# Kernel tuning notes

Hardware: AMD Instinct MI355X
Metric: run time of the kernel (lower is better)

The kernel has to match this reference:

```python
import jax, jax.numpy as jnp
import numpy as np

H, DK, DV, DM = 8, 64, 64, 512
B, LQ, LK = 8, 512, 1024
NEG = -1e30  # stand-in for -inf (avoids NaN under masking)


def setup_inputs() -> dict:
    key = jax.random.key(0)
    ks = jax.random.split(key, 12)
    s = 0.04  # ~xavier scale for 512x512
    return {
        "q": jax.random.normal(ks[0], (B, LQ, DM), jnp.float32),
        "k": jax.random.normal(ks[1], (B, LK, DM), jnp.float32),
        "v": jax.random.normal(ks[2], (B, LK, DM), jnp.float32),
        "w_qs": jax.random.normal(ks[3], (DM, H * DK), jnp.float32) * s,
        "w_ks": jax.random.normal(ks[4], (DM, H * DK), jnp.float32) * s,
        "w_vs": jax.random.normal(ks[5], (DM, H * DV), jnp.float32) * s,
        "w_fc": jax.random.normal(ks[6], (H * DV, DM), jnp.float32) * s,
        "key_mask": (jax.random.uniform(ks[7], (B, LQ, LK)) > 0.1).astype(jnp.float32),
        "query_mask": (jax.random.uniform(ks[8], (B, LQ, 1)) > 0.1).astype(jnp.float32),
        "mapping_mask": (jax.random.uniform(ks[9], (B, LQ, LK)) > 0.1).astype(jnp.float32),
        "attn_prior": jax.random.uniform(ks[10], (B, LK, LQ), jnp.float32),  # [B, Lk, Lq]
    }


def reference(q, k, v, w_qs, w_ks, w_vs, w_fc, key_mask, query_mask, mapping_mask, attn_prior):
    residual = q
    # projections -> [H, B, L, d]
    qh = (q @ w_qs).reshape(B, LQ, H, DK).transpose(2, 0, 1, 3)
    kh = (k @ w_ks).reshape(B, LK, H, DK).transpose(2, 0, 1, 3)
    vh = (v @ w_vs).reshape(B, LK, H, DV).transpose(2, 0, 1, 3)
    # scaled scores [H, B, Lq, Lk]
    attn = jnp.einsum('hbqd,hbkd->hbqk', qh, kh) / jnp.sqrt(jnp.float32(DK))
    attn = jnp.where(key_mask[None] == 0.0, NEG, attn)
    # fuse log-prior into log-domain scores
    attn = jax.nn.log_softmax(attn, axis=-1) + jnp.log(attn_prior.transpose(0, 2, 1)[None] + 1e-8)
    attn_logprob = attn[:, :, None]  # [H, B, 1, Lq, Lk]
    p = jax.nn.softmax(attn, axis=-1)
    p = p * query_mask[None]
    attn_raw = p
    p = p * mapping_mask[None]
    out = jnp.einsum('hbqk,hbkd->hbqd', p, vh)          # [H, B, Lq, dv]
    out = out.transpose(1, 2, 0, 3).reshape(B, LQ, H * DV)
    out = out @ w_fc + residual                          # dropout=0.0
    return (out, p, attn_raw, attn_logprob)
```

## Files before the change

### kernel.cpp

```cpp
#include <hip/hip_runtime.h>

#define H   8
#define DK  64
#define DV  64
#define DM  512
#define B_  8
#define LQ  512
#define LK  1024
#define NEG (-1e30f)

typedef __attribute__((ext_vector_type(8))) short bf16x8;
typedef __attribute__((ext_vector_type(4))) float f32x4;

__device__ __forceinline__ short f2bf(float f) {
    union { float f; unsigned u; } x; x.f = f;
    unsigned r = x.u + 0x7fffu + ((x.u >> 16) & 1u);
    return (short)(r >> 16);
}
__device__ __forceinline__ unsigned pack2(float a, float b) {
    return (unsigned)(unsigned short)f2bf(a) | ((unsigned)(unsigned short)f2bf(b) << 16);
}
__device__ __forceinline__ float bflo(unsigned w) {
    union { unsigned u; float f; } x; x.u = w << 16; return x.f;
}
__device__ __forceinline__ float bfhi(unsigned w) {
    union { unsigned u; float f; } x; x.u = w & 0xFFFF0000u; return x.f;
}
__device__ __forceinline__ unsigned pkh(float a, float b) {
    union { _Float16 h[2]; unsigned u; } x;
    x.h[0] = (_Float16)a; x.h[1] = (_Float16)b; return x.u;
}
__device__ __forceinline__ float uph(unsigned w, int i) {
    union { unsigned u; _Float16 h[2]; } x; x.u = w;
    return (float)x.h[i];
}

__global__ __launch_bounds__(256) void prep_kernel(
    const float* __restrict__ wqs, const float* __restrict__ wks,
    const float* __restrict__ wvs, const float* __restrict__ wfc,
    const float* __restrict__ prior, const float* __restrict__ km,
    const float* __restrict__ mm, short* __restrict__ WT,
    short* __restrict__ prtb, unsigned short* __restrict__ kmbits,
    unsigned short* __restrict__ mmbits) {
    __shared__ float tile[64][65];
    int bx = blockIdx.x;
    int t = threadIdx.x;
    if (bx < 1024) {
        int mat = bx >> 8, tt = bx & 255;
        int k0 = (tt >> 4) * 32, n0 = (tt & 15) * 32;
        int tx = t & 31, ty = t >> 5;
        const float* src = (mat == 0) ? wqs : (mat == 1) ? wks : (mat == 2) ? wvs : wfc;
        short* dst = WT + (size_t)mat * DM * DM;
#pragma unroll
        for (int i = 0; i < 4; i++)
            tile[ty + i * 8][tx] = src[(size_t)(k0 + ty + i * 8) * DM + n0 + tx];
        __syncthreads();
#pragma unroll
        for (int i = 0; i < 4; i++)
            dst[(size_t)(n0 + ty + i * 8) * DM + k0 + tx] = f2bf(tile[tx][ty + i * 8]);
    } else if (bx < 2048) {
        int tt = bx - 1024;
        int b = tt >> 7, rem = tt & 127;
        int k0 = (rem >> 3) * 64, q0 = (rem & 7) * 64;
        int tx = t & 63, ty = t >> 6;
        const float* src = prior + (size_t)b * LK * LQ;
        short* dst = prtb + (size_t)b * LQ * LK;
#pragma unroll
        for (int i = 0; i < 16; i++)
            tile[ty + i * 4][tx] = src[(size_t)(k0 + ty + i * 4) * LQ + q0 + tx];
        __syncthreads();
#pragma unroll
        for (int i = 0; i < 16; i++)
            dst[(size_t)(q0 + ty + i * 4) * LK + k0 + tx] = f2bf(tile[tx][ty + i * 4] + 1e-8f);
    } else {
        int rr = (bx - 2048) * 4 + (t >> 6);
        int lane = t & 63;
        const float* kmr = km + (size_t)rr * LK;
        const float* mmr = mm + (size_t)rr * LK;
        unsigned kb = 0, mb = 0;
#pragma unroll
        for (int c = 0; c < 4; c++) {
            float4 k4 = *(const float4*)(kmr + c * 256 + lane * 4);
            float4 m4 = *(const float4*)(mmr + c * 256 + lane * 4);
            kb |= (unsigned)(k4.x != 0.f) << (c * 4 + 0);
            kb |= (unsigned)(k4.y != 0.f) << (c * 4 + 1);
            kb |= (unsigned)(k4.z != 0.f) << (c * 4 + 2);
            kb |= (unsigned)(k4.w != 0.f) << (c * 4 + 3);
            mb |= (unsigned)(m4.x != 0.f) << (c * 4 + 0);
            mb |= (unsigned)(m4.y != 0.f) << (c * 4 + 1);
            mb |= (unsigned)(m4.z != 0.f) << (c * 4 + 2);
            mb |= (unsigned)(m4.w != 0.f) << (c * 4 + 3);
        }
        kmbits[(size_t)rr * 64 + lane] = (unsigned short)kb;
        mmbits[(size_t)rr * 64 + lane] = (unsigned short)mb;
    }
}

__global__ __launch_bounds__(256) void proj_all(
    const float* __restrict__ Xq, const float* __restrict__ Xk,
    const float* __restrict__ Xv, const short* __restrict__ WT,
    short* __restrict__ QHb, short* __restrict__ KHb, short* __restrict__ VT) {
    int bx = blockIdx.x;
    const float* X; const short* W; short* out; int mode, r0;
    if (bx < 64)       { X = Xq; W = WT;          out = QHb; mode = 0; r0 = bx * 64; }
    else if (bx < 192) { X = Xk; W = WT + 262144; out = KHb; mode = 0; r0 = (bx - 64) * 64; }
    else               { X = Xv; W = WT + 524288; out = VT;  mode = 1; r0 = (bx - 192) * 64; }
    int tid = threadIdx.x;
    int wid = tid >> 6, lane = tid & 63, g = lane >> 4, ln = lane & 15;
    int wr = wid >> 1, wc = wid & 1;
    int cb = blockIdx.y * 256;
    f32x4 acc[4][2][2] = {};
    for (int kb = 0; kb < 16; kb++) {
        bf16x8 a[2];
#pragma unroll
        for (int i = 0; i < 2; i++) {
            int row = r0 + wr * 32 + i * 16 + ln;
            const float* xp = X + (size_t)row * DM + kb * 32 + g * 8;
            float4 x0 = *(const float4*)xp;
            float4 x1 = *(const float4*)(xp + 4);
            bf16x8 av;
            av[0] = f2bf(x0.x); av[1] = f2bf(x0.y); av[2] = f2bf(x0.z); av[3] = f2bf(x0.w);
            av[4] = f2bf(x1.x); av[5] = f2bf(x1.y); av[6] = f2bf(x1.z); av[7] = f2bf(x1.w);
            a[i] = av;
        }
#pragma unroll
        for (int cc = 0; cc < 4; cc++) {
            bf16x8 b[2];
#pragma unroll
            for (int j = 0; j < 2; j++) {
                int col = cb + cc * 64 + wc * 32 + j * 16 + ln;
                b[j] = *(const bf16x8*)(W + (size_t)col * DM + kb * 32 + g * 8);
            }
#pragma unroll
            for (int i = 0; i < 2; i++)
#pragma unroll
                for (int j = 0; j < 2; j++)
                    acc[cc][i][j] = __builtin_amdgcn_mfma_f32_16x16x32_bf16(a[i], b[j], acc[cc][i][j], 0, 0, 0);
        }
    }
#pragma unroll
    for (int cc = 0; cc < 4; cc++)
#pragma unroll
        for (int i = 0; i < 2; i++)
#pragma unroll
            for (int j = 0; j < 2; j++) {
                int colg = cb + cc * 64 + wc * 32 + j * 16 + ln;
                if (mode == 0) {
#pragma unroll
                    for (int r = 0; r < 4; r++) {
                        int rowg = r0 + wr * 32 + i * 16 + g * 4 + r;
                        out[(size_t)rowg * DM + colg] = f2bf(acc[cc][i][j][r]);
                    }
                } else {
                    int hh = colg >> 6, d = colg & 63;
                    int rbase = r0 + wr * 32 + i * 16 + g * 4;
                    int bb = rbase >> 10, kk = rbase & 1023;
                    union { short s[4]; unsigned long long u; } pk;
#pragma unroll
                    for (int r = 0; r < 4; r++) pk.s[r] = f2bf(acc[cc][i][j][r]);
                    *(unsigned long long*)(out + ((size_t)((hh * B_ + bb) * DV + d)) * LK + kk) = pk.u;
                }
            }
}

#define SROWB 2064
__global__ __launch_bounds__(512, 6) void attn_kernel(
    const short* __restrict__ QHb, const short* __restrict__ KHb,
    const short* __restrict__ VT, const short* __restrict__ prtb,
    const unsigned short* __restrict__ kmbits, const unsigned short* __restrict__ mmbits,
    const float* __restrict__ qm, float* __restrict__ p_out,
    float* __restrict__ raw_out, float* __restrict__ lgp_out,
    short* __restrict__ outh) {
    __shared__ char lds[16 * SROWB];
    int tid = threadIdx.x;
    int wid = tid >> 6, lane = tid & 63, g = lane >> 4, ln = lane & 15;
    int q0 = blockIdx.x * 16, b = blockIdx.y, h = blockIdx.z;
    int kw0 = wid * 128;
    int row0 = wid * 2;
    const size_t rb0 = (size_t)(b * LQ + q0 + row0);

    unsigned kmb[2], mmb[2];
    float qmv[2];
    uint2 prW[2][4];
#pragma unroll
    for (int rr = 0; rr < 2; rr++) {
        kmb[rr] = kmbits[(rb0 + rr) * 64 + lane];
        mmb[rr] = mmbits[(rb0 + rr) * 64 + lane];
        qmv[rr] = qm[rb0 + rr];
#pragma unroll
        for (int c = 0; c < 4; c++)
            prW[rr][c] = *(const uint2*)(prtb + (rb0 + rr) * LK + c * 256 + lane * 4);
    }

    bf16x8 bq0, bq1;
    {
        const short* qp = QHb + ((size_t)(b * LQ + q0 + ln)) * DM + h * DK + g * 8;
        bq0 = *(const bf16x8*)qp;
        bq1 = *(const bf16x8*)(qp + 32);
    }
#pragma unroll
    for (int kt = 0; kt < 8; kt++) {
        int k0 = kw0 + kt * 16;
        const short* kp = KHb + ((size_t)(b * LK + k0 + ln)) * DM + h * DK + g * 8;
        bf16x8 ak0 = *(const bf16x8*)kp;
        bf16x8 ak1 = *(const bf16x8*)(kp + 32);
        f32x4 sa = {0.f, 0.f, 0.f, 0.f};
        sa = __builtin_amdgcn_mfma_f32_16x16x32_bf16(ak0, bq0, sa, 0, 0, 0);
        sa = __builtin_amdgcn_mfma_f32_16x16x32_bf16(ak1, bq1, sa, 0, 0, 0);
        uint2 sp;
        sp.x = pkh(sa[0], sa[1]);
        sp.y = pkh(sa[2], sa[3]);
        *(uint2*)(lds + ln * SROWB + (k0 + g * 4) * 2) = sp;
    }
    __syncthreads();

    float s1[2] = {0.f, 0.f}, s2[2] = {0.f, 0.f};
    uint2 xc[2][4];
#pragma unroll
    for (int rr = 0; rr < 2; rr++) {
        const char* svp = lds + (row0 + rr) * SROWB;
#pragma unroll
        for (int c = 0; c < 4; c++) {
            int e0 = c * 256 + lane * 4;
            uint2 prv = prW[rr][c];
            uint2 sp = *(const uint2*)(svp + e0 * 2);
            float sv[4] = { uph(sp.x, 0), uph(sp.x, 1), uph(sp.y, 0), uph(sp.y, 1) };
            float pr[4] = { bflo(prv.x), bfhi(prv.x), bflo(prv.y), bfhi(prv.y) };
            float xr[4];
#pragma unroll
            for (int r = 0; r < 4; r++) {
                float kmf = (float)((kmb[rr] >> (c * 4 + r)) & 1u);
                float e = kmf * __expf(sv[r] * 0.125f - 16.0f);
                float x = e * pr[r];
                s1[rr] += e;
                s2[rr] += x;
                xr[r] = x;
            }
            xc[rr][c].x = pack2(xr[0], xr[1]);
            xc[rr][c].y = pack2(xr[2], xr[3]);
        }
    }
#pragma unroll
    for (int m = 1; m < 64; m <<= 1) {
        s1[0] += __shfl_xor(s1[0], m, 64);
        s1[1] += __shfl_xor(s1[1], m, 64);
        s2[0] += __shfl_xor(s2[0], m, 64);
        s2[1] += __shfl_xor(s2[1], m, 64);
    }

#pragma unroll
    for (int rr = 0; rr < 2; rr++) {
        float inv1 = 1.0f / s1[rr];
        float inv2 = 1.0f / s2[rr];
        const size_t ob = ((size_t)((h * B_ + b) * LQ + q0 + row0 + rr)) * LK;
        short* pfp = (short*)(lds + (row0 + rr) * SROWB);
#pragma unroll
        for (int c = 0; c < 4; c++) {
            int e0 = c * 256 + lane * 4;
            float xv[4] = { bflo(xc[rr][c].x), bfhi(xc[rr][c].x),
                            bflo(xc[rr][c].y), bfhi(xc[rr][c].y) };
            f32x4 pw, rw, lw;
            union { short s[4]; unsigned long long u; } pk;
#pragma unroll
            for (int r = 0; r < 4; r++) {
                float mmf = (float)((mmb[rr] >> (c * 4 + r)) & 1u);
                float xr = xv[r];
                float p0 = xr * inv2;
                float praw = p0 * qmv[rr];
                float pfin = praw * mmf;
                float lgp = fmaxf(__logf(xr * inv1), -1e30f);
                pw[r] = pfin;
                rw[r] = praw;
                lw[r] = lgp;
                pk.s[r] = f2bf(pfin);
            }
            __builtin_nontemporal_store(pw, (f32x4*)(p_out + ob + e0));
            __builtin_nontemporal_store(rw, (f32x4*)(raw_out + ob + e0));
            __builtin_nontemporal_store(lw, (f32x4*)(lgp_out + ob + e0));
            *(unsigned long long*)(pfp + e0) = pk.u;
        }
    }
    __syncthreads();

    if (wid >= 4) return;
    f32x4 oacc = {0.f, 0.f, 0.f, 0.f};
    int d0 = wid * 16;
    const short* vrow = VT + ((size_t)((h * B_ + b) * DV + d0 + ln)) * LK;
    const short* prow = (const short*)(lds + ln * SROWB);
    for (int kc = 0; kc < 32; kc++) {
        bf16x8 ap = *(const bf16x8*)(prow + kc * 32 + g * 8);
        bf16x8 bv = *(const bf16x8*)(vrow + kc * 32 + g * 8);
        oacc = __builtin_amdgcn_mfma_f32_16x16x32_bf16(ap, bv, oacc, 0, 0, 0);
    }
#pragma unroll
    for (int r = 0; r < 4; r++) {
        int row = q0 + g * 4 + r;
        outh[((size_t)(b * LQ + row)) * DM + h * DV + d0 + ln] = f2bf(oacc[r]);
    }
}

__global__ __launch_bounds__(256) void final_kernel(
    const short* __restrict__ outh, const short* __restrict__ WTfc,
    const float* __restrict__ qres, float* __restrict__ out) {
    int tid = threadIdx.x;
    int wid = tid >> 6, lane = tid & 63, g = lane >> 4, ln = lane & 15;
    int wr = wid >> 1, wc = wid & 1;
    int r0 = blockIdx.x * 64, c0 = blockIdx.y * 64;
    f32x4 acc[2][2] = {};
    for (int kb = 0; kb < 16; kb++) {
        bf16x8 a[2], b[2];
#pragma unroll
        for (int i = 0; i < 2; i++)
            a[i] = *(const bf16x8*)(outh + ((size_t)(r0 + wr * 32 + i * 16 + ln)) * DM + kb * 32 + g * 8);
#pragma unroll
        for (int j = 0; j < 2; j++)
            b[j] = *(const bf16x8*)(WTfc + ((size_t)(c0 + wc * 32 + j * 16 + ln)) * DM + kb * 32 + g * 8);
#pragma unroll
        for (int i = 0; i < 2; i++)
#pragma unroll
            for (int j = 0; j < 2; j++)
                acc[i][j] = __builtin_amdgcn_mfma_f32_16x16x32_bf16(a[i], b[j], acc[i][j], 0, 0, 0);
    }
#pragma unroll
    for (int i = 0; i < 2; i++)
#pragma unroll
        for (int j = 0; j < 2; j++)
#pragma unroll
            for (int r = 0; r < 4; r++) {
                int row = r0 + wr * 32 + i * 16 + g * 4 + r;
                int col = c0 + wc * 32 + j * 16 + ln;
                float v = acc[i][j][r] + qres[(size_t)row * DM + col];
                __builtin_nontemporal_store(v, out + (size_t)row * DM + col);
            }
}

extern "C" void kernel_launch(void* const* d_in, const int* in_sizes, int n_in,
                              void* d_out, int out_size, void* d_ws, size_t ws_size,
                              hipStream_t stream) {
    (void)in_sizes; (void)n_in; (void)out_size; (void)ws_size;
    const float* q     = (const float*)d_in[0];
    const float* k     = (const float*)d_in[1];
    const float* v     = (const float*)d_in[2];
    const float* wqs   = (const float*)d_in[3];
    const float* wks   = (const float*)d_in[4];
    const float* wvs   = (const float*)d_in[5];
    const float* wfc   = (const float*)d_in[6];
    const float* km    = (const float*)d_in[7];
    const float* qm    = (const float*)d_in[8];
    const float* mm    = (const float*)d_in[9];
    const float* prior = (const float*)d_in[10];

    char* ws = (char*)d_ws;
    short* WT               = (short*)(ws);
    short* QHb              = (short*)(ws + 2097152);
    short* KHb              = (short*)(ws + 6291456);
    short* VT               = (short*)(ws + 14680064);
    short* prtb             = (short*)(ws + 23068672);
    short* outh             = (short*)(ws + 31457280);
    unsigned short* kmbits  = (unsigned short*)(ws + 35651584);
    unsigned short* mmbits  = (unsigned short*)(ws + 36175872);

    float* out     = (float*)d_out;
    float* p_out   = out + 2097152;
    float* raw_out = p_out + 33554432;
    float* lgp_out = raw_out + 33554432;

    prep_kernel<<<dim3(3072), dim3(256), 0, stream>>>(wqs, wks, wvs, wfc, prior, km, mm,
                                                      WT, prtb, kmbits, mmbits);
    proj_all<<<dim3(320, 2), 256, 0, stream>>>(q, k, v, WT, QHb, KHb, VT);
    attn_kernel<<<dim3(32, 8, 8), dim3(512), 0, stream>>>(QHb, KHb, VT, prtb, kmbits, mmbits,
                                                          qm, p_out, raw_out, lgp_out, outh);
    final_kernel<<<dim3(64, 8), 256, 0, stream>>>(outh, WT + 786432, q, out);
}
```

Baseline: 201.2 us.

## Move prior transpose and mask packing into projection kernel; use lighter LDS barriers

Result: no change. 199.2 us (-1.0%).

```diff
diff --git a/kernel.cpp b/kernel.cpp
--- a/kernel.cpp
+++ b/kernel.cpp
@@ -34,46 +34,46 @@
     union { unsigned u; _Float16 h[2]; } x; x.u = w;
     return (float)x.h[i];
 }
+__device__ __forceinline__ void bar_lds() {
+    asm volatile("s_waitcnt lgkmcnt(0)" ::: "memory");
+    __builtin_amdgcn_s_barrier();
+}
 
 __global__ __launch_bounds__(256) void prep_kernel(
     const float* __restrict__ wqs, const float* __restrict__ wks,
     const float* __restrict__ wvs, const float* __restrict__ wfc,
+    short* __restrict__ WT) {
+    __shared__ float tile[32][33];
+    int bx = blockIdx.x;
+    int t = threadIdx.x;
+    int mat = bx >> 8, tt = bx & 255;
+    int k0 = (tt >> 4) * 32, n0 = (tt & 15) * 32;
+    int tx = t & 31, ty = t >> 5;
+    const float* src = (mat == 0) ? wqs : (mat == 1) ? wks : (mat == 2) ? wvs : wfc;
+    short* dst = WT + (size_t)mat * DM * DM;
+#pragma unroll
+    for (int i = 0; i < 4; i++)
+        tile[ty + i * 8][tx] = src[(size_t)(k0 + ty + i * 8) * DM + n0 + tx];
+    __syncthreads();
+#pragma unroll
+    for (int i = 0; i < 4; i++)
+        dst[(size_t)(n0 + ty + i * 8) * DM + k0 + tx] = f2bf(tile[tx][ty + i * 8]);
+}
+
+__global__ __launch_bounds__(256) void proj_all(
+    const float* __restrict__ Xq, const float* __restrict__ Xk,
+    const float* __restrict__ Xv, const short* __restrict__ WT,
     const float* __restrict__ prior, const float* __restrict__ km,
-    const float* __restrict__ mm, short* __restrict__ WT,
+    const float* __restrict__ mm,
+    short* __restrict__ QHb, short* __restrict__ KHb, short* __restrict__ VT,
     short* __restrict__ prtb, unsigned short* __restrict__ kmbits,
     unsigned short* __restrict__ mmbits) {
     __shared__ float tile[64][65];
     int bx = blockIdx.x;
     int t = threadIdx.x;
-    if (bx < 1024) {
-        int mat = bx >> 8, tt = bx & 255;
-        int k0 = (tt >> 4) * 32, n0 = (tt & 15) * 32;
-        int tx = t & 31, ty = t >> 5;
-        const float* src = (mat == 0) ? wqs : (mat == 1) ? wks : (mat == 2) ? wvs : wfc;
-        short* dst = WT + (size_t)mat * DM * DM;
-#pragma unroll
-        for (int i = 0; i < 4; i++)
-            tile[ty + i * 8][tx] = src[(size_t)(k0 + ty + i * 8) * DM + n0 + tx];
-        __syncthreads();
-#pragma unroll
-        for (int i = 0; i < 4; i++)
-            dst[(size_t)(n0 + ty + i * 8) * DM + k0 + tx] = f2bf(tile[tx][ty + i * 8]);
-    } else if (bx < 2048) {
-        int tt = bx - 1024;
-        int b = tt >> 7, rem = tt & 127;
-        int k0 = (rem >> 3) * 64, q0 = (rem & 7) * 64;
-        int tx = t & 63, ty = t >> 6;
-        const float* src = prior + (size_t)b * LK * LQ;
-        short* dst = prtb + (size_t)b * LQ * LK;
-#pragma unroll
-        for (int i = 0; i < 16; i++)
-            tile[ty + i * 4][tx] = src[(size_t)(k0 + ty + i * 4) * LQ + q0 + tx];
-        __syncthreads();
-#pragma unroll
-        for (int i = 0; i < 16; i++)
-            dst[(size_t)(q0 + ty + i * 4) * LK + k0 + tx] = f2bf(tile[tx][ty + i * 4] + 1e-8f);
-    } else {
-        int rr = (bx - 2048) * 4 + (t >> 6);
+    if (bx >= 1344) {
+        if (blockIdx.y != 0) return;
+        int rr = (bx - 1344) * 4 + (t >> 6);
         int lane = t & 63;
         const float* kmr = km + (size_t)rr * LK;
         const float* mmr = mm + (size_t)rr * LK;
@@ -93,14 +93,25 @@
         }
         kmbits[(size_t)rr * 64 + lane] = (unsigned short)kb;
         mmbits[(size_t)rr * 64 + lane] = (unsigned short)mb;
-    }
-}
-
-__global__ __launch_bounds__(256) void proj_all(
-    const float* __restrict__ Xq, const float* __restrict__ Xk,
-    const float* __restrict__ Xv, const short* __restrict__ WT,
-    short* __restrict__ QHb, short* __restrict__ KHb, short* __restrict__ VT) {
-    int bx = blockIdx.x;
+        return;
+    }
+    if (bx >= 320) {
+        if (blockIdx.y != 0) return;
+        int tt = bx - 320;
+        int b = tt >> 7, rem = tt & 127;
+        int k0 = (rem >> 3) * 64, q0 = (rem & 7) * 64;
+        int tx = t & 63, ty = t >> 6;
+        const float* src = prior + (size_t)b * LK * LQ;
+        short* dst = prtb + (size_t)b * LQ * LK;
+#pragma unroll
+        for (int i = 0; i < 16; i++)
+            tile[ty + i * 4][tx] = src[(size_t)(k0 + ty + i * 4) * LQ + q0 + tx];
+        __syncthreads();
+#pragma unroll
+        for (int i = 0; i < 16; i++)
+            dst[(size_t)(q0 + ty + i * 4) * LK + k0 + tx] = f2bf(tile[tx][ty + i * 4] + 1e-8f);
+        return;
+    }
     const float* X; const short* W; short* out; int mode, r0;
     if (bx < 64)       { X = Xq; W = WT;          out = QHb; mode = 0; r0 = bx * 64; }
     else if (bx < 192) { X = Xk; W = WT + 262144; out = KHb; mode = 0; r0 = (bx - 64) * 64; }
@@ -212,7 +223,7 @@
         sp.y = pkh(sa[2], sa[3]);
         *(uint2*)(lds + ln * SROWB + (k0 + g * 4) * 2) = sp;
     }
-    __syncthreads();
+    bar_lds();
 
     float s1[2] = {0.f, 0.f}, s2[2] = {0.f, 0.f};
     uint2 xc[2][4];
@@ -280,7 +291,7 @@
             *(unsigned long long*)(pfp + e0) = pk.u;
         }
     }
-    __syncthreads();
+    bar_lds();
 
     if (wid >= 4) return;
     f32x4 oacc = {0.f, 0.f, 0.f, 0.f};
@@ -365,9 +376,9 @@
     float* raw_out = p_out + 33554432;
     float* lgp_out = raw_out + 33554432;
 
-    prep_kernel<<<dim3(3072), dim3(256), 0, stream>>>(wqs, wks, wvs, wfc, prior, km, mm,
-                                                      WT, prtb, kmbits, mmbits);
-    proj_all<<<dim3(320, 2), 256, 0, stream>>>(q, k, v, WT, QHb, KHb, VT);
+    prep_kernel<<<dim3(1024), dim3(256), 0, stream>>>(wqs, wks, wvs, wfc, WT);
+    proj_all<<<dim3(2368, 2), 256, 0, stream>>>(q, k, v, WT, prior, km, mm,
+                                                QHb, KHb, VT, prtb, kmbits, mmbits);
     attn_kernel<<<dim3(32, 8, 8), dim3(512), 0, stream>>>(QHb, KHb, VT, prtb, kmbits, mmbits,
                                                           qm, p_out, raw_out, lgp_out, outh);
     final_kernel<<<dim3(64, 8), 256, 0, stream>>>(outh, WT + 786432, q, out);
```
